# Performance work log

Measured on AMD Instinct MI355X. Metric: run time of the kernel, lower is better.

The kernel has to match this reference:

```python
import jax, jax.numpy as jnp
import numpy as np

D_IN = 1024
D_MODEL = 1024
NUM_HEADS = 16
DEPTH = D_MODEL // NUM_HEADS


def setup_inputs() -> dict:
    key = jax.random.key(0)
    ks = jax.random.split(key, 7)
    B, N = 2, 2048
    s = 1.0 / np.sqrt(D_IN)
    return {
        "x": jax.random.normal(ks[0], (B, N, D_IN), dtype=jnp.float32),
        "Wq": jax.random.normal(ks[1], (D_IN, D_MODEL), dtype=jnp.float32) * s,
        "bq": jnp.zeros((D_MODEL,), dtype=jnp.float32),
        "Wk": jax.random.normal(ks[2], (D_IN, D_MODEL), dtype=jnp.float32) * s,
        "bk": jnp.zeros((D_MODEL,), dtype=jnp.float32),
        "Wv": jax.random.normal(ks[3], (D_IN, D_MODEL), dtype=jnp.float32) * s,
        "bv": jnp.zeros((D_MODEL,), dtype=jnp.float32),
    }


def _split_heads(t):
    B, N, _ = t.shape
    return t.reshape(B, N, NUM_HEADS, DEPTH).transpose(0, 2, 1, 3)  # [B,H,N,depth]


def reference(x, Wq, bq, Wk, bk, Wv, bv):
    B, N, _ = x.shape
    q = _split_heads(x @ Wq + bq)
    k = _split_heads(x @ Wk + bk)
    v = _split_heads(x @ Wv + bv)
    scale = 1.0 / jnp.sqrt(jnp.float32(DEPTH))
    attn = jnp.einsum("bhnd,bhmd->bhnm", q, k) * scale  # [B,H,N,N]
    attn = jax.nn.softmax(attn, axis=-1)
    out = jnp.einsum("bhnm,bhmd->bhnd", attn, v)
    return out.transpose(0, 2, 1, 3).reshape(B, N, D_MODEL)
```

## Files before the change

kernel.cpp:

```cpp
#include <hip/hip_runtime.h>
#include <cstdint>


#define SEQ_N 2048
#define NHEAD 16
#define DEPTH 64
#define SCALE_Q (0.125f * 1.44269504088896340736f)
#define M_OFF (-12.0f)

typedef short bf16x8 __attribute__((ext_vector_type(8)));
typedef short short4v __attribute__((ext_vector_type(4)));
typedef float f32x4 __attribute__((ext_vector_type(4)));

#define MFMA32(a, b, c) __builtin_amdgcn_mfma_f32_16x16x32_bf16((a), (b), (c), 0, 0, 0)

#if defined(__has_builtin)
#if __has_builtin(__builtin_amdgcn_exp2f)
#define FEXP2(x) __builtin_amdgcn_exp2f(x)
#endif
#endif
#ifndef FEXP2
#define FEXP2(x) exp2f(x)
#endif

__device__ __forceinline__ short f2b(float f) {
    union { float f; unsigned u; } v; v.f = f;
    unsigned u = v.u;
    return (short)((u + 0x7FFFu + ((u >> 16) & 1u)) >> 16);
}

__device__ __forceinline__ unsigned cvt_pk_bf16(float lo, float hi) {
    unsigned r;
    asm("v_cvt_pk_bf16_f32 %0, %1, %2" : "=v"(r) : "v"(lo), "v"(hi));
    return r;
}

__device__ __forceinline__ void gld_lds16(const void* g, void* l) {
    __builtin_amdgcn_global_load_lds(
        (const __attribute__((address_space(1))) unsigned int*)(uintptr_t)g,
        (__attribute__((address_space(3))) unsigned int*)(uintptr_t)l, 16, 0, 0);
}

__global__ __launch_bounds__(256) void cvt_all_kernel(
    const float* __restrict__ x, short* __restrict__ xb,
    const float* __restrict__ Wq, const float* __restrict__ Wk,
    const float* __restrict__ Wv, short* __restrict__ WT)
{
    __shared__ float tile[64][65];
    if (blockIdx.x < 2048) {
        const int i = blockIdx.x * 256 + threadIdx.x;
        const float4* xi = (const float4*)x + (size_t)i * 2;
        const float4 a = xi[0], c = xi[1];
        bf16x8 o;
        o[0] = f2b(a.x); o[1] = f2b(a.y); o[2] = f2b(a.z); o[3] = f2b(a.w);
        o[4] = f2b(c.x); o[5] = f2b(c.y); o[6] = f2b(c.z); o[7] = f2b(c.w);
        *((bf16x8*)xb + i) = o;
        return;
    }
    const int bid = blockIdx.x - 2048;
    const int mat = bid >> 8;
    const int t = bid & 255;
    const int k0 = (t >> 4) * 64, n0 = (t & 15) * 64;
    const float* W = (mat == 0) ? Wq : ((mat == 1) ? Wk : Wv);
    const int tt = threadIdx.x;
#pragma unroll
    for (int i = 0; i < 16; ++i) {
        const int idx = tt + i * 256;
        const int r = idx >> 6, c = idx & 63;
        tile[r][c] = W[(size_t)(k0 + r) * 1024 + n0 + c];
    }
    __syncthreads();
#pragma unroll
    for (int i = 0; i < 16; ++i) {
        const int idx = tt + i * 256;
        const int r = idx >> 6, c = idx & 63;
        WT[(size_t)(mat * 1024 + n0 + r) * 1024 + k0 + c] = f2b(tile[c][r]);
    }
}

__global__ __launch_bounds__(512, 2) void qkv_gemm_kernel(
    const short* __restrict__ A, const short* __restrict__ BT,
    const float* __restrict__ bq, const float* __restrict__ bk, const float* __restrict__ bv,
    short* __restrict__ Qb, short* __restrict__ Kb, short* __restrict__ VTb)
{
    __shared__ __align__(16) short sm[57344];
    const int tid = threadIdx.x;
    const int l = tid & 63, w = tid >> 6;
    const int lr = l & 15, lk = l >> 4;
    const int wr = w >> 2, wcn = w & 3;

    const int id2 = (blockIdx.x & 7) * 32 + (blockIdx.x >> 3);
    const int bm = id2 & 15, bn = id2 >> 4;
    const int row0 = bm * 256, col0 = bn * 192;

    const int gsrc8 = ((tid & 7) ^ ((tid >> 3) & 7)) << 3;
    const short* a_src = A + (size_t)(row0 + (tid >> 3)) * 1024 + gsrc8;
    const short* b_src = BT + (size_t)(col0 + (tid >> 3)) * 1024 + gsrc8;

    const int aBase = (wr * 128 + lr) * 64;
    const int bBase = (wcn * 48 + lr) * 64;
    const int asw0 = ((lk)     ^ (lr & 7)) << 3;
    const int asw1 = ((lk + 4) ^ (lr & 7)) << 3;

    f32x4 acc[8][3];
#pragma unroll
    for (int m = 0; m < 8; ++m)
#pragma unroll
        for (int n = 0; n < 3; ++n) acc[m][n] = (f32x4){0.f, 0.f, 0.f, 0.f};

    gld_lds16(a_src,          sm + tid * 8);
    gld_lds16(a_src + 65536,  sm + tid * 8 + 4096);
    gld_lds16(a_src + 131072, sm + tid * 8 + 8192);
    gld_lds16(a_src + 196608, sm + tid * 8 + 12288);
    gld_lds16(b_src,          sm + 32768 + tid * 8);
    gld_lds16(b_src + 65536,  sm + 32768 + tid * 8 + 4096);
    gld_lds16(b_src + 131072, sm + 32768 + tid * 8 + 8192);

#define PHASE(P, GLDS)                                                          \
    do {                                                                        \
        bf16x8 af[2][2];                                                        \
        af[0][0] = *(const bf16x8*)(Al + aBase + (2*(P))*1024 + asw0);          \
        af[0][1] = *(const bf16x8*)(Al + aBase + (2*(P))*1024 + asw1);          \
        af[1][0] = *(const bf16x8*)(Al + aBase + (2*(P)+1)*1024 + asw0);        \
        af[1][1] = *(const bf16x8*)(Al + aBase + (2*(P)+1)*1024 + asw1);        \
        GLDS;                                                                   \
        __builtin_amdgcn_s_barrier();                                           \
        asm volatile("s_waitcnt lgkmcnt(0)" ::: "memory");                      \
        __builtin_amdgcn_sched_barrier(0);                                      \
        __builtin_amdgcn_s_setprio(1);                                          \
        _Pragma("unroll")                                                       \
        for (int mm = 0; mm < 2; ++mm)                                          \
            _Pragma("unroll")                                                   \
            for (int n = 0; n < 3; ++n) {                                       \
                acc[2*(P)+mm][n] = MFMA32(af[mm][0], bfv[n][0], acc[2*(P)+mm][n]); \
                acc[2*(P)+mm][n] = MFMA32(af[mm][1], bfv[n][1], acc[2*(P)+mm][n]); \
            }                                                                   \
        __builtin_amdgcn_s_setprio(0);                                          \
        __builtin_amdgcn_s_barrier();                                           \
    } while (0)

#pragma unroll 2
    for (int kt = 0; kt < 16; ++kt) {
        const int cur = kt & 1, nxt = cur ^ 1;
        const short* Al = sm + cur * 16384;
        const short* Bl = sm + 32768 + cur * 12288;
        short* And = sm + nxt * 16384;
        short* Bnd = sm + 32768 + nxt * 12288;
        const int k1 = (kt + 1) * 64;
        const bool more = (kt < 15);

        bf16x8 bfv[3][2];

        if (more) {
            gld_lds16(a_src + k1,         And + tid * 8);
            gld_lds16(a_src + k1 + 65536, And + tid * 8 + 4096);
            asm volatile("s_waitcnt vmcnt(2)" ::: "memory");
        } else {
            asm volatile("s_waitcnt vmcnt(0)" ::: "memory");
        }
        __builtin_amdgcn_s_barrier();
        __builtin_amdgcn_sched_barrier(0);
        {
            bf16x8 af[2][2];
            af[0][0] = *(const bf16x8*)(Al + aBase + asw0);
            af[0][1] = *(const bf16x8*)(Al + aBase + asw1);
            af[1][0] = *(const bf16x8*)(Al + aBase + 1024 + asw0);
            af[1][1] = *(const bf16x8*)(Al + aBase + 1024 + asw1);
#pragma unroll
            for (int n = 0; n < 3; ++n) {
                bfv[n][0] = *(const bf16x8*)(Bl + bBase + n * 1024 + asw0);
                bfv[n][1] = *(const bf16x8*)(Bl + bBase + n * 1024 + asw1);
            }
            asm volatile("s_waitcnt lgkmcnt(0)" ::: "memory");
            __builtin_amdgcn_sched_barrier(0);
            __builtin_amdgcn_s_setprio(1);
#pragma unroll
            for (int mm = 0; mm < 2; ++mm)
#pragma unroll
                for (int n = 0; n < 3; ++n) {
                    acc[mm][n] = MFMA32(af[mm][0], bfv[n][0], acc[mm][n]);
                    acc[mm][n] = MFMA32(af[mm][1], bfv[n][1], acc[mm][n]);
                }
            __builtin_amdgcn_s_setprio(0);
        }
        __builtin_amdgcn_s_barrier();

        PHASE(1, if (more) { gld_lds16(a_src + k1 + 131072, And + tid * 8 + 8192);
                             gld_lds16(a_src + k1 + 196608, And + tid * 8 + 12288); });
        PHASE(2, if (more) { gld_lds16(b_src + k1,          Bnd + tid * 8);
                             gld_lds16(b_src + k1 + 65536,  Bnd + tid * 8 + 4096); });
        PHASE(3, if (more) { gld_lds16(b_src + k1 + 131072, Bnd + tid * 8 + 8192); });
    }
#undef PHASE

    short* Cl = sm;
#pragma unroll
    for (int n = 0; n < 3; ++n) {
        const int gb = col0 + wcn * 48 + n * 16;
        const int mat = gb >> 10;
        const int jj = (gb + lr) & 1023;
        if (mat < 2) {
            const float bias = ((mat == 0) ? bq : bk)[jj];
            const float sc = (mat == 0) ? SCALE_Q : 1.0f;
            const int cc = wcn * 48 + n * 16 + lr;
#pragma unroll
            for (int m = 0; m < 8; ++m) {
                const int rbase = wr * 128 + m * 16 + lk * 4;
#pragma unroll
                for (int r = 0; r < 4; ++r)
                    Cl[(rbase + r) * 200 + cc] = f2b((acc[m][n][r] + bias) * sc);
            }
        } else {
            const float bias = bv[jj];
            const int h = jj >> 6, d = jj & 63;
#pragma unroll
            for (int m = 0; m < 8; ++m) {
                const int grow0 = row0 + wr * 128 + m * 16 + lk * 4;
                const int bb = grow0 >> 11, ns0 = grow0 & 2047;
                const int g = (ns0 >> 2) & 15;
                const int gp = (g & 8) | ((g & 3) << 1) | ((g >> 2) & 1);
                const int nsp = (ns0 & ~63) | (gp << 2);
                short4v pv;
#pragma unroll
                for (int r = 0; r < 4; ++r) pv[r] = f2b(acc[m][n][r] + bias);
                *(short4v*)(VTb + ((size_t)(bb * NHEAD + h) * DEPTH + d) * SEQ_N + nsp) = pv;
            }
        }
    }
    __syncthreads();
    {
        const int row = tid >> 1, half = tid & 1;
        const int grow = row0 + row;
        const int bb = grow >> 11, ns = grow & 2047;
#pragma unroll
        for (int i = 0; i < 12; ++i) {
            const int cc = half * 96 + i * 8;
            const int gc = col0 + cc;
            const int mat = gc >> 10;
            if (mat < 2) {
                short* O = mat ? Kb : Qb;
                const int h = (gc & 1023) >> 6, d0 = gc & 63;
                *(bf16x8*)(O + ((size_t)(bb * NHEAD + h) * SEQ_N + ns) * DEPTH + d0) =
                    *(const bf16x8*)(Cl + row * 200 + cc);
            }
        }
    }
}


__device__ __forceinline__ float exppack32_lane(const f32x4 s[4], bf16x8 pb[2]) {
    float rs = 0.f;
#pragma unroll
    for (int kk = 0; kk < 2; ++kk) {
        union { unsigned u[4]; bf16x8 v; } pk;
#pragma unroll
        for (int hh = 0; hh < 2; ++hh) {
            const int c = 2 * kk + hh;
            const float p0 = FEXP2(s[c][0]);
            const float p1 = FEXP2(s[c][1]);
            const float p2 = FEXP2(s[c][2]);
            const float p3 = FEXP2(s[c][3]);
            rs += (p0 + p1) + (p2 + p3);
            pk.u[2 * hh]     = cvt_pk_bf16(p0, p1);
            pk.u[2 * hh + 1] = cvt_pk_bf16(p2, p3);
        }
        pb[kk] = pk.v;
    }
    return rs;
}

#define NT 16

__global__ __launch_bounds__(256, 2) void attn_kernel(
    const short* __restrict__ Qb, const short* __restrict__ Kb,
    const short* __restrict__ VTb, float* __restrict__ out)
{
    __shared__ short smem[2][16384];

    const int tid = threadIdx.x;
    const int l = tid & 63, w = tid >> 6;
    const int lr = l & 15, lk = l >> 4;

    const int hb = blockIdx.x;
    const int slot = hb >> 3;
    const int bh = (hb & 7) * 4 + (slot >> 4);
    const int qt = slot & 15;
    const int b = bh >> 4, h = bh & 15;

    const int qw = qt * 128 + w * 32;

    const short* Qg = Qb + ((size_t)bh * SEQ_N + qw + lr) * DEPTH + lk * 8;
    const bf16x8 bq00 = *(const bf16x8*)(Qg);
    const bf16x8 bq01 = *(const bf16x8*)(Qg + 32);
    const bf16x8 bq10 = *(const bf16x8*)(Qg + 16 * DEPTH);
    const bf16x8 bq11 = *(const bf16x8*)(Qg + 16 * DEPTH + 32);

    const short* Kg = Kb + (size_t)bh * SEQ_N * DEPTH;
    const short* Vg = VTb + (size_t)bh * DEPTH * SEQ_N;

    const int srow = tid >> 3;
    const int sg = (tid & 7) ^ (srow & 7);
    const short* Ksrc = Kg + (size_t)srow * DEPTH + sg * 8;
    const short* Vsrc = Vg + (size_t)srow * SEQ_N + sg * 8;

#define STAGE(BUF, T)                                                            \
    do {                                                                         \
        const int key0_ = (T) * 128;                                             \
        short* dst = &smem[BUF][w * 512];                                        \
        gld_lds16(Ksrc + (size_t)key0_ * DEPTH, dst);                            \
        gld_lds16(Ksrc + (size_t)(key0_ + 32) * DEPTH, dst + 2048);              \
        gld_lds16(Ksrc + (size_t)(key0_ + 64) * DEPTH, dst + 4096);              \
        gld_lds16(Ksrc + (size_t)(key0_ + 96) * DEPTH, dst + 6144);              \
        gld_lds16(Vsrc + key0_, dst + 8192);                                     \
        gld_lds16(Vsrc + key0_ + 32 * SEQ_N, dst + 10240);                       \
        gld_lds16(Vsrc + key0_ + 64, dst + 12288);                               \
        gld_lds16(Vsrc + key0_ + 64 + 32 * SEQ_N, dst + 14336);                  \
    } while (0)

    const short* s0p = &smem[0][0];
    const int aoff0 = lr * 64 + (((lk    ) ^ (lr & 7)) << 3);
    const int aoff1 = lr * 64 + (((lk + 4) ^ (lr & 7)) << 3);

    f32x4 acc0[4], acc1[4];
#pragma unroll
    for (int n = 0; n < 4; ++n) {
        acc0[n] = (f32x4){0.f, 0.f, 0.f, 0.f};
        acc1[n] = (f32x4){0.f, 0.f, 0.f, 0.f};
    }
    float l0 = 0.f, l1 = 0.f;

    STAGE(0, 0);
    asm volatile("s_waitcnt vmcnt(0)" ::: "memory");
    __builtin_amdgcn_s_barrier();
    __builtin_amdgcn_sched_barrier(0);

#pragma unroll 2
    for (int t = 0; t < NT; ++t) {
        const int cur = t & 1;
        const int tn = (t + 1 < NT) ? (t + 1) : (NT - 1);
        STAGE(cur ^ 1, tn);

#pragma unroll
        for (int ss = 0; ss < 2; ++ss) {
            const int sub = ss ^ (w & 1);
            const short* Kl = s0p + cur * 16384 + sub * 4096;
            const short* Vl = Kl + 8192;

            bf16x8 kf[4][2], vf[4][2];
#pragma unroll
            for (int c = 0; c < 4; ++c) {
                kf[c][0] = *(const bf16x8*)(Kl + c * 1024 + aoff0);
                kf[c][1] = *(const bf16x8*)(Kl + c * 1024 + aoff1);
            }
#pragma unroll
            for (int n = 0; n < 4; ++n) {
                vf[n][0] = *(const bf16x8*)(Vl + n * 1024 + aoff0);
                vf[n][1] = *(const bf16x8*)(Vl + n * 1024 + aoff1);
            }

            f32x4 s0[4], s1[4];
            __builtin_amdgcn_s_setprio(1);
#pragma unroll
            for (int c = 0; c < 4; ++c) {
                f32x4 a = (f32x4){M_OFF, M_OFF, M_OFF, M_OFF};
                a = MFMA32(kf[c][0], bq00, a);
                a = MFMA32(kf[c][1], bq01, a);
                s0[c] = a;
                f32x4 bb2 = (f32x4){M_OFF, M_OFF, M_OFF, M_OFF};
                bb2 = MFMA32(kf[c][0], bq10, bb2);
                bb2 = MFMA32(kf[c][1], bq11, bb2);
                s1[c] = bb2;
            }
            __builtin_amdgcn_s_setprio(0);

            bf16x8 pb0[2], pb1[2];
            l0 += exppack32_lane(s0, pb0);
            l1 += exppack32_lane(s1, pb1);

            __builtin_amdgcn_s_setprio(1);
#pragma unroll
            for (int n = 0; n < 4; ++n) {
                acc0[n] = MFMA32(vf[n][0], pb0[0], acc0[n]);
                acc0[n] = MFMA32(vf[n][1], pb0[1], acc0[n]);
                acc1[n] = MFMA32(vf[n][0], pb1[0], acc1[n]);
                acc1[n] = MFMA32(vf[n][1], pb1[1], acc1[n]);
            }
            __builtin_amdgcn_s_setprio(0);
        }

        asm volatile("s_waitcnt vmcnt(0)" ::: "memory");
        __builtin_amdgcn_s_barrier();
        __builtin_amdgcn_sched_barrier(0);
    }
#undef STAGE

    l0 += __shfl_xor(l0, 16); l0 += __shfl_xor(l0, 32);
    l1 += __shfl_xor(l1, 16); l1 += __shfl_xor(l1, 32);

    const float inv0 = 1.0f / l0, inv1 = 1.0f / l1;
    float* o0 = out + ((size_t)b * SEQ_N + qw + lr) * 1024 + h * 64 + lk * 4;
    float* o1 = o0 + (size_t)16 * 1024;
#pragma unroll
    for (int n = 0; n < 4; ++n) {
        const f32x4 v0 = acc0[n] * inv0;
        const f32x4 v1 = acc1[n] * inv1;
        *(f32x4*)(o0 + n * 16) = v0;
        *(f32x4*)(o1 + n * 16) = v1;
    }
}

extern "C" void kernel_launch(void* const* d_in, const int* in_sizes, int n_in,
                              void* d_out, int out_size, void* d_ws, size_t ws_size,
                              hipStream_t stream) {
    const float* x  = (const float*)d_in[0];
    const float* Wq = (const float*)d_in[1];
    const float* bq = (const float*)d_in[2];
    const float* Wk = (const float*)d_in[3];
    const float* bk = (const float*)d_in[4];
    const float* Wv = (const float*)d_in[5];
    const float* bv = (const float*)d_in[6];
    float* out = (float*)d_out;

    char* ws = (char*)d_ws;
    short* xb  = (short*)(ws);
    short* WT  = (short*)(ws + (8  << 20));
    short* Qb  = (short*)(ws + (14 << 20));
    short* Kb  = (short*)(ws + (22 << 20));
    short* VTb = (short*)(ws + (30 << 20));

    cvt_all_kernel<<<2816, 256, 0, stream>>>(x, xb, Wq, Wk, Wv, WT);
    qkv_gemm_kernel<<<256, 512, 0, stream>>>(xb, WT, bq, bk, bv, Qb, Kb, VTb);
    attn_kernel<<<512, 256, 0, stream>>>(Qb, Kb, VTb, out);
}
```

Baseline: 82.49 us.

## Split attention keys across warp pairs with 64-row query tiles per warp

```diff
diff --git a/kernel.cpp b/kernel.cpp
--- a/kernel.cpp
+++ b/kernel.cpp
@@ -77,6 +77,8 @@
         WT[(size_t)(mat * 1024 + n0 + r) * 1024 + k0 + c] = f2b(tile[c][r]);
     }
 }
+
+#define GEMM_K 1024
 
 __global__ __launch_bounds__(512, 2) void qkv_gemm_kernel(
     const short* __restrict__ A, const short* __restrict__ BT,
@@ -269,17 +271,18 @@
     return rs;
 }
 
-#define NT 16
+#define NTK 16
 
 __global__ __launch_bounds__(256, 2) void attn_kernel(
     const short* __restrict__ Qb, const short* __restrict__ Kb,
     const short* __restrict__ VTb, float* __restrict__ out)
 {
-    __shared__ short smem[2][16384];
+    __shared__ __align__(16) short smem[2][2][8192];
 
     const int tid = threadIdx.x;
     const int l = tid & 63, w = tid >> 6;
     const int lr = l & 15, lk = l >> 4;
+    const int qh = w & 1, kh = w >> 1;
 
     const int hb = blockIdx.x;
     const int slot = hb >> 3;
@@ -287,13 +290,15 @@
     const int qt = slot & 15;
     const int b = bh >> 4, h = bh & 15;
 
-    const int qw = qt * 128 + w * 32;
+    const int qw = qt * 128 + qh * 64;
 
     const short* Qg = Qb + ((size_t)bh * SEQ_N + qw + lr) * DEPTH + lk * 8;
-    const bf16x8 bq00 = *(const bf16x8*)(Qg);
-    const bf16x8 bq01 = *(const bf16x8*)(Qg + 32);
-    const bf16x8 bq10 = *(const bf16x8*)(Qg + 16 * DEPTH);
-    const bf16x8 bq11 = *(const bf16x8*)(Qg + 16 * DEPTH + 32);
+    bf16x8 bq[4][2];
+#pragma unroll
+    for (int g = 0; g < 4; ++g) {
+        bq[g][0] = *(const bf16x8*)(Qg + g * 16 * DEPTH);
+        bq[g][1] = *(const bf16x8*)(Qg + g * 16 * DEPTH + 32);
+    }
 
     const short* Kg = Kb + (size_t)bh * SEQ_N * DEPTH;
     const short* Vg = VTb + (size_t)bh * DEPTH * SEQ_N;
@@ -303,31 +308,30 @@
     const short* Ksrc = Kg + (size_t)srow * DEPTH + sg * 8;
     const short* Vsrc = Vg + (size_t)srow * SEQ_N + sg * 8;
 
-#define STAGE(BUF, T)                                                            \
-    do {                                                                         \
-        const int key0_ = (T) * 128;                                             \
-        short* dst = &smem[BUF][w * 512];                                        \
-        gld_lds16(Ksrc + (size_t)key0_ * DEPTH, dst);                            \
-        gld_lds16(Ksrc + (size_t)(key0_ + 32) * DEPTH, dst + 2048);              \
-        gld_lds16(Ksrc + (size_t)(key0_ + 64) * DEPTH, dst + 4096);              \
-        gld_lds16(Ksrc + (size_t)(key0_ + 96) * DEPTH, dst + 6144);              \
-        gld_lds16(Vsrc + key0_, dst + 8192);                                     \
-        gld_lds16(Vsrc + key0_ + 32 * SEQ_N, dst + 10240);                       \
-        gld_lds16(Vsrc + key0_ + 64, dst + 12288);                               \
-        gld_lds16(Vsrc + key0_ + 64 + 32 * SEQ_N, dst + 14336);                  \
+#define STAGE(BUF, T)                                                             \
+    do {                                                                          \
+        const int ko_ = (T) * 64;                                                 \
+        short* d0 = &smem[BUF][0][w * 512];                                       \
+        short* d1 = &smem[BUF][1][w * 512];                                       \
+        gld_lds16(Ksrc + (size_t)ko_ * DEPTH, d0);                                \
+        gld_lds16(Ksrc + (size_t)(ko_ + 32) * DEPTH, d0 + 2048);                  \
+        gld_lds16(Vsrc + ko_, d0 + 4096);                                         \
+        gld_lds16(Vsrc + ko_ + 32 * SEQ_N, d0 + 6144);                            \
+        gld_lds16(Ksrc + (size_t)(1024 + ko_) * DEPTH, d1);                       \
+        gld_lds16(Ksrc + (size_t)(1024 + ko_ + 32) * DEPTH, d1 + 2048);           \
+        gld_lds16(Vsrc + 1024 + ko_, d1 + 4096);                                  \
+        gld_lds16(Vsrc + 1024 + ko_ + 32 * SEQ_N, d1 + 6144);                     \
     } while (0)
 
-    const short* s0p = &smem[0][0];
     const int aoff0 = lr * 64 + (((lk    ) ^ (lr & 7)) << 3);
     const int aoff1 = lr * 64 + (((lk + 4) ^ (lr & 7)) << 3);
 
-    f32x4 acc0[4], acc1[4];
-#pragma unroll
-    for (int n = 0; n < 4; ++n) {
-        acc0[n] = (f32x4){0.f, 0.f, 0.f, 0.f};
-        acc1[n] = (f32x4){0.f, 0.f, 0.f, 0.f};
-    }
-    float l0 = 0.f, l1 = 0.f;
+    f32x4 acc[4][4];
+#pragma unroll
+    for (int g = 0; g < 4; ++g)
+#pragma unroll
+        for (int n = 0; n < 4; ++n) acc[g][n] = (f32x4){0.f, 0.f, 0.f, 0.f};
+    float lsum[4] = {0.f, 0.f, 0.f, 0.f};
 
     STAGE(0, 0);
     asm volatile("s_waitcnt vmcnt(0)" ::: "memory");
@@ -335,55 +339,47 @@
     __builtin_amdgcn_sched_barrier(0);
 
 #pragma unroll 2
-    for (int t = 0; t < NT; ++t) {
+    for (int t = 0; t < NTK; ++t) {
         const int cur = t & 1;
-        const int tn = (t + 1 < NT) ? (t + 1) : (NT - 1);
+        const int tn = (t + 1 < NTK) ? (t + 1) : (NTK - 1);
         STAGE(cur ^ 1, tn);
 
-#pragma unroll
-        for (int ss = 0; ss < 2; ++ss) {
-            const int sub = ss ^ (w & 1);
-            const short* Kl = s0p + cur * 16384 + sub * 4096;
-            const short* Vl = Kl + 8192;
-
-            bf16x8 kf[4][2], vf[4][2];
-#pragma unroll
-            for (int c = 0; c < 4; ++c) {
-                kf[c][0] = *(const bf16x8*)(Kl + c * 1024 + aoff0);
-                kf[c][1] = *(const bf16x8*)(Kl + c * 1024 + aoff1);
-            }
-#pragma unroll
-            for (int n = 0; n < 4; ++n) {
-                vf[n][0] = *(const bf16x8*)(Vl + n * 1024 + aoff0);
-                vf[n][1] = *(const bf16x8*)(Vl + n * 1024 + aoff1);
-            }
-
-            f32x4 s0[4], s1[4];
+        const short* Kl = &smem[cur][kh][0];
+        const short* Vl = Kl + 4096;
+
+        bf16x8 kf[4][2], vf[4][2];
+#pragma unroll
+        for (int c = 0; c < 4; ++c) {
+            kf[c][0] = *(const bf16x8*)(Kl + c * 1024 + aoff0);
+            kf[c][1] = *(const bf16x8*)(Kl + c * 1024 + aoff1);
+        }
+#pragma unroll
+        for (int n = 0; n < 4; ++n) {
+            vf[n][0] = *(const bf16x8*)(Vl + n * 1024 + aoff0);
+            vf[n][1] = *(const bf16x8*)(Vl + n * 1024 + aoff1);
+        }
+
+#pragma unroll
+        for (int g = 0; g < 4; ++g) {
+            f32x4 s[4];
             __builtin_amdgcn_s_setprio(1);
 #pragma unroll
             for (int c = 0; c < 4; ++c) {
                 f32x4 a = (f32x4){M_OFF, M_OFF, M_OFF, M_OFF};
-                a = MFMA32(kf[c][0], bq00, a);
-                a = MFMA32(kf[c][1], bq01, a);
-                s0[c] = a;
-                f32x4 bb2 = (f32x4){M_OFF, M_OFF, M_OFF, M_OFF};
-                bb2 = MFMA32(kf[c][0], bq10, bb2);
-                bb2 = MFMA32(kf[c][1], bq11, bb2);
-                s1[c] = bb2;
+                a = MFMA32(kf[c][0], bq[g][0], a);
+                a = MFMA32(kf[c][1], bq[g][1], a);
+                s[c] = a;
             }
             __builtin_amdgcn_s_setprio(0);
 
-            bf16x8 pb0[2], pb1[2];
-            l0 += exppack32_lane(s0, pb0);
-            l1 += exppack32_lane(s1, pb1);
+            bf16x8 pb[2];
+            lsum[g] += exppack32_lane(s, pb);
 
             __builtin_amdgcn_s_setprio(1);
 #pragma unroll
             for (int n = 0; n < 4; ++n) {
-                acc0[n] = MFMA32(vf[n][0], pb0[0], acc0[n]);
-                acc0[n] = MFMA32(vf[n][1], pb0[1], acc0[n]);
-                acc1[n] = MFMA32(vf[n][0], pb1[0], acc1[n]);
-                acc1[n] = MFMA32(vf[n][1], pb1[1], acc1[n]);
+                acc[g][n] = MFMA32(vf[n][0], pb[0], acc[g][n]);
+                acc[g][n] = MFMA32(vf[n][1], pb[1], acc[g][n]);
             }
             __builtin_amdgcn_s_setprio(0);
         }
@@ -394,18 +390,38 @@
     }
 #undef STAGE
 
-    l0 += __shfl_xor(l0, 16); l0 += __shfl_xor(l0, 32);
-    l1 += __shfl_xor(l1, 16); l1 += __shfl_xor(l1, 32);
-
-    const float inv0 = 1.0f / l0, inv1 = 1.0f / l1;
-    float* o0 = out + ((size_t)b * SEQ_N + qw + lr) * 1024 + h * 64 + lk * 4;
-    float* o1 = o0 + (size_t)16 * 1024;
-#pragma unroll
-    for (int n = 0; n < 4; ++n) {
-        const f32x4 v0 = acc0[n] * inv0;
-        const f32x4 v1 = acc1[n] * inv1;
-        *(f32x4*)(o0 + n * 16) = v0;
-        *(f32x4*)(o1 + n * 16) = v1;
+#pragma unroll
+    for (int g = 0; g < 4; ++g) {
+        lsum[g] += __shfl_xor(lsum[g], 16);
+        lsum[g] += __shfl_xor(lsum[g], 32);
+    }
+
+    float* fsm = (float*)&smem[0][0][0];
+    const int pbase = qh * 4416;
+    if (kh == 1) {
+#pragma unroll
+        for (int g = 0; g < 4; ++g)
+#pragma unroll
+            for (int n = 0; n < 4; ++n)
+                *(f32x4*)(fsm + pbase + (g * 16 + lr) * 68 + n * 16 + lk * 4) = acc[g][n];
+        if (lk == 0) {
+#pragma unroll
+            for (int g = 0; g < 4; ++g) fsm[pbase + 4352 + g * 16 + lr] = lsum[g];
+        }
+    }
+    __syncthreads();
+    if (kh == 0) {
+#pragma unroll
+        for (int g = 0; g < 4; ++g) {
+            const float lt = lsum[g] + fsm[pbase + 4352 + g * 16 + lr];
+            const float inv = 1.0f / lt;
+            float* o = out + ((size_t)b * SEQ_N + qw + g * 16 + lr) * 1024 + h * 64 + lk * 4;
+#pragma unroll
+            for (int n = 0; n < 4; ++n) {
+                const f32x4 p = *(const f32x4*)(fsm + pbase + (g * 16 + lr) * 68 + n * 16 + lk * 4);
+                *(f32x4*)(o + n * 16) = (acc[g][n] + p) * inv;
+            }
+        }
     }
 }
 
```

Result: no change. 83.27 us (+0.9%).

## Replace four-phase interleaved QKV GEMM mainloop with simple whole-tile double buffering

Applied to the files above, without the earlier changes.

```diff
diff --git a/kernel.cpp b/kernel.cpp
--- a/kernel.cpp
+++ b/kernel.cpp
@@ -108,90 +108,57 @@
 #pragma unroll
         for (int n = 0; n < 3; ++n) acc[m][n] = (f32x4){0.f, 0.f, 0.f, 0.f};
 
-    gld_lds16(a_src,          sm + tid * 8);
-    gld_lds16(a_src + 65536,  sm + tid * 8 + 4096);
-    gld_lds16(a_src + 131072, sm + tid * 8 + 8192);
-    gld_lds16(a_src + 196608, sm + tid * 8 + 12288);
-    gld_lds16(b_src,          sm + 32768 + tid * 8);
-    gld_lds16(b_src + 65536,  sm + 32768 + tid * 8 + 4096);
-    gld_lds16(b_src + 131072, sm + 32768 + tid * 8 + 8192);
-
-#define PHASE(P, GLDS)                                                          \
-    do {                                                                        \
-        bf16x8 af[2][2];                                                        \
-        af[0][0] = *(const bf16x8*)(Al + aBase + (2*(P))*1024 + asw0);          \
-        af[0][1] = *(const bf16x8*)(Al + aBase + (2*(P))*1024 + asw1);          \
-        af[1][0] = *(const bf16x8*)(Al + aBase + (2*(P)+1)*1024 + asw0);        \
-        af[1][1] = *(const bf16x8*)(Al + aBase + (2*(P)+1)*1024 + asw1);        \
-        GLDS;                                                                   \
-        __builtin_amdgcn_s_barrier();                                           \
-        asm volatile("s_waitcnt lgkmcnt(0)" ::: "memory");                      \
-        __builtin_amdgcn_sched_barrier(0);                                      \
-        __builtin_amdgcn_s_setprio(1);                                          \
-        _Pragma("unroll")                                                       \
-        for (int mm = 0; mm < 2; ++mm)                                          \
-            _Pragma("unroll")                                                   \
-            for (int n = 0; n < 3; ++n) {                                       \
-                acc[2*(P)+mm][n] = MFMA32(af[mm][0], bfv[n][0], acc[2*(P)+mm][n]); \
-                acc[2*(P)+mm][n] = MFMA32(af[mm][1], bfv[n][1], acc[2*(P)+mm][n]); \
-            }                                                                   \
-        __builtin_amdgcn_s_setprio(0);                                          \
-        __builtin_amdgcn_s_barrier();                                           \
+#define GSTAGE(BUF, KT)                                                    \
+    do {                                                                   \
+        short* asb = sm + (BUF) * 16384;                                   \
+        short* bsb = sm + 32768 + (BUF) * 12288;                           \
+        gld_lds16(a_src + (KT) * 64,          &asb[tid * 8]);              \
+        gld_lds16(a_src + (KT) * 64 + 65536,  &asb[tid * 8 + 4096]);       \
+        gld_lds16(a_src + (KT) * 64 + 131072, &asb[tid * 8 + 8192]);       \
+        gld_lds16(a_src + (KT) * 64 + 196608, &asb[tid * 8 + 12288]);      \
+        gld_lds16(b_src + (KT) * 64,          &bsb[tid * 8]);              \
+        gld_lds16(b_src + (KT) * 64 + 65536,  &bsb[tid * 8 + 4096]);       \
+        gld_lds16(b_src + (KT) * 64 + 131072, &bsb[tid * 8 + 8192]);       \
     } while (0)
+
+    GSTAGE(0, 0);
 
 #pragma unroll 2
     for (int kt = 0; kt < 16; ++kt) {
-        const int cur = kt & 1, nxt = cur ^ 1;
+        const int cur = kt & 1;
+        if (kt + 1 < 16) {
+            GSTAGE(cur ^ 1, kt + 1);
+            asm volatile("s_waitcnt vmcnt(7)" ::: "memory");
+        } else {
+            asm volatile("s_waitcnt vmcnt(0)" ::: "memory");
+        }
+        __builtin_amdgcn_s_barrier();
+        __builtin_amdgcn_sched_barrier(0);
+
         const short* Al = sm + cur * 16384;
         const short* Bl = sm + 32768 + cur * 12288;
-        short* And = sm + nxt * 16384;
-        short* Bnd = sm + 32768 + nxt * 12288;
-        const int k1 = (kt + 1) * 64;
-        const bool more = (kt < 15);
 
         bf16x8 bfv[3][2];
-
-        if (more) {
-            gld_lds16(a_src + k1,         And + tid * 8);
-            gld_lds16(a_src + k1 + 65536, And + tid * 8 + 4096);
-            asm volatile("s_waitcnt vmcnt(2)" ::: "memory");
-        } else {
-            asm volatile("s_waitcnt vmcnt(0)" ::: "memory");
-        }
+#pragma unroll
+        for (int n = 0; n < 3; ++n) {
+            bfv[n][0] = *(const bf16x8*)(Bl + bBase + n * 1024 + asw0);
+            bfv[n][1] = *(const bf16x8*)(Bl + bBase + n * 1024 + asw1);
+        }
+#pragma unroll
+        for (int m = 0; m < 8; ++m) {
+            bf16x8 a0 = *(const bf16x8*)(Al + aBase + m * 1024 + asw0);
+            bf16x8 a1 = *(const bf16x8*)(Al + aBase + m * 1024 + asw1);
+#pragma unroll
+            for (int n = 0; n < 3; ++n) {
+                acc[m][n] = MFMA32(a0, bfv[n][0], acc[m][n]);
+                acc[m][n] = MFMA32(a1, bfv[n][1], acc[m][n]);
+            }
+        }
+
+        __builtin_amdgcn_sched_barrier(0);
         __builtin_amdgcn_s_barrier();
-        __builtin_amdgcn_sched_barrier(0);
-        {
-            bf16x8 af[2][2];
-            af[0][0] = *(const bf16x8*)(Al + aBase + asw0);
-            af[0][1] = *(const bf16x8*)(Al + aBase + asw1);
-            af[1][0] = *(const bf16x8*)(Al + aBase + 1024 + asw0);
-            af[1][1] = *(const bf16x8*)(Al + aBase + 1024 + asw1);
-#pragma unroll
-            for (int n = 0; n < 3; ++n) {
-                bfv[n][0] = *(const bf16x8*)(Bl + bBase + n * 1024 + asw0);
-                bfv[n][1] = *(const bf16x8*)(Bl + bBase + n * 1024 + asw1);
-            }
-            asm volatile("s_waitcnt lgkmcnt(0)" ::: "memory");
-            __builtin_amdgcn_sched_barrier(0);
-            __builtin_amdgcn_s_setprio(1);
-#pragma unroll
-            for (int mm = 0; mm < 2; ++mm)
-#pragma unroll
-                for (int n = 0; n < 3; ++n) {
-                    acc[mm][n] = MFMA32(af[mm][0], bfv[n][0], acc[mm][n]);
-                    acc[mm][n] = MFMA32(af[mm][1], bfv[n][1], acc[mm][n]);
-                }
-            __builtin_amdgcn_s_setprio(0);
-        }
-        __builtin_amdgcn_s_barrier();
-
-        PHASE(1, if (more) { gld_lds16(a_src + k1 + 131072, And + tid * 8 + 8192);
-                             gld_lds16(a_src + k1 + 196608, And + tid * 8 + 12288); });
-        PHASE(2, if (more) { gld_lds16(b_src + k1,          Bnd + tid * 8);
-                             gld_lds16(b_src + k1 + 65536,  Bnd + tid * 8 + 4096); });
-        PHASE(3, if (more) { gld_lds16(b_src + k1 + 131072, Bnd + tid * 8 + 8192); });
-    }
-#undef PHASE
+    }
+#undef GSTAGE
 
     short* Cl = sm;
 #pragma unroll
```

After: 83.72 us. Within noise of the previous version (+1.5%).
